# Kernel optimization log

Measured on AMD Instinct MI355X. Metric: run time of the kernel, lower is better.

## Reference

```python
import jax, jax.numpy as jnp
import numpy as np


def setup_inputs() -> dict:
    key = jax.random.key(0)
    k0, k1, k2, k3, k4 = jax.random.split(key, 5)
    T, B, I, H = 1024, 128, 256, 256
    x = jax.random.normal(k0, (T, B, I), dtype=jnp.float32)
    h0 = jax.random.normal(k1, (1, B, H), dtype=jnp.float32)
    # prepacked transposed weights, gate order [r|z|n] along the 3H axis
    wihT = jax.random.normal(k2, (I, 3 * H), dtype=jnp.float32) * 0.05
    whhT = jax.random.normal(k3, (H, 3 * H), dtype=jnp.float32) * 0.05
    b = jax.random.normal(k4, (3 * H,), dtype=jnp.float32) * 0.05  # fused b_ih + b_hh
    return {"x": x, "h0": h0, "wihT": wihT, "whhT": whhT, "b": b}


def reference(x, h0, wihT, whhT, b):
    # Single-layer GRU recurrence, matching the fused CUDA kernel math:
    #   r = sigmoid(x Wir + h Whr + b_r)
    #   z = sigmoid(x Wiz + h Whz + b_z)
    #   h' = (1 - z) * n + z * h
    H = h0.shape[-1]
    br, bz, bn = b[:H], b[H:2 * H], b[2 * H:]

    def step(h, xt):
        gi = xt @ wihT   # (B, 3H)
        gh = h @ whhT    # (B, 3H)
        r = jax.nn.sigmoid(gi[:, :H] + gh[:, :H] + br)
        z = jax.nn.sigmoid(gi[:, H:2 * H] + gh[:, H:2 * H] + bz)
        n = jnp.tanh(gi[:, 2 * H:] + bn + r * gh[:, 2 * H:])
        h_new = (1.0 - z) * n + z * h
        return h_new, None

    h_final, _ = jax.lax.scan(step, h0[0], x)  # scan over T
    return h_final[None]  # (1, B, H)
```

## Files before the change

kernel.cpp:

```cpp
#include <hip/hip_runtime.h>
#include <hip/hip_fp16.h>

#define TT 1024
#define BB 128
#define II 256
#define HH 256
#define NG 768

__device__ __align__(16) unsigned short g_xbf[(size_t)TT * BB * II];
__device__ __align__(16) unsigned short g_wihB[NG * II];
__device__ __align__(16) _Float16       g_gi[(size_t)TT * BB * NG];

typedef __attribute__((ext_vector_type(8))) short    bfrag;
typedef __attribute__((ext_vector_type(8))) _Float16 hfrag;
typedef __attribute__((ext_vector_type(4))) float    f32x4;

__device__ __forceinline__ unsigned short f2bf(float f) {
    unsigned u = __float_as_uint(f);
    return (unsigned short)((u + 0x7fffu + ((u >> 16) & 1u)) >> 16);
}

__global__ void cvt_x_kernel(const float* __restrict__ x) {
    const int n4 = TT * BB * II / 4;
    for (int i = blockIdx.x * blockDim.x + threadIdx.x; i < n4;
         i += gridDim.x * blockDim.x) {
        float4 v = reinterpret_cast<const float4*>(x)[i];
        ushort4 o;
        o.x = f2bf(v.x); o.y = f2bf(v.y); o.z = f2bf(v.z); o.w = f2bf(v.w);
        reinterpret_cast<ushort4*>(g_xbf)[i] = o;
    }
}

__global__ void cvt_wih_kernel(const float* __restrict__ wihT) {
    const int n = blockIdx.x;
    const int k = threadIdx.x;
    g_wihB[n * II + k] = f2bf(wihT[k * NG + n]);
}

__global__ void __launch_bounds__(256) gi_gemm_kernel(const float* __restrict__ bias) {
    __shared__ unsigned short Ab[128 * 32];
    __shared__ unsigned short Bb[128 * 32];
    const int tid = threadIdx.x;
    const int mt = blockIdx.x / 6, nt = blockIdx.x % 6;
    const int m0 = mt * 128, n0 = nt * 128;
    const int l = tid & 63, w = tid >> 6;
    const int wr = w >> 1, wc = w & 1;
    const int srow = tid >> 2, scol = (tid & 3) * 8;

    f32x4 acc[4][4] = {};

    for (int ks = 0; ks < 8; ++ks) {
        const int k0 = ks * 32;
        __syncthreads();
        #pragma unroll
        for (int c = 0; c < 2; ++c) {
            const int row = c * 64 + srow;
            *reinterpret_cast<uint4*>(&Ab[row * 32 + scol]) =
                *reinterpret_cast<const uint4*>(&g_xbf[(size_t)(m0 + row) * II + k0 + scol]);
            *reinterpret_cast<uint4*>(&Bb[row * 32 + scol]) =
                *reinterpret_cast<const uint4*>(&g_wihB[(n0 + row) * II + k0 + scol]);
        }
        __syncthreads();
        bfrag af[4], bf[4];
        #pragma unroll
        for (int i = 0; i < 4; ++i) {
            af[i] = *reinterpret_cast<const bfrag*>(
                        &Ab[(wr * 64 + i * 16 + (l & 15)) * 32 + (l >> 4) * 8]);
            bf[i] = *reinterpret_cast<const bfrag*>(
                        &Bb[(wc * 64 + i * 16 + (l & 15)) * 32 + (l >> 4) * 8]);
        }
        #pragma unroll
        for (int mi = 0; mi < 4; ++mi)
            #pragma unroll
            for (int ni = 0; ni < 4; ++ni)
                acc[mi][ni] = __builtin_amdgcn_mfma_f32_16x16x32_bf16(
                                  af[mi], bf[ni], acc[mi][ni], 0, 0, 0);
    }
    #pragma unroll
    for (int mi = 0; mi < 4; ++mi) {
        const int grow = m0 + wr * 64 + mi * 16 + (l >> 4) * 4;
        #pragma unroll
        for (int ni = 0; ni < 4; ++ni) {
            const int gcol = n0 + wc * 64 + ni * 16 + (l & 15);
            const float bv = bias[gcol];
            #pragma unroll
            for (int q = 0; q < 4; ++q)
                g_gi[(size_t)(grow + q) * NG + gcol] = (_Float16)(acc[mi][ni][q] + bv);
        }
    }
}

#define MF(A, B, C) __builtin_amdgcn_mfma_f32_16x16x32_f16((A), (B), (C), 0, 0, 0)

#define LDB1(NAME, CB, KT)                                                  \
    hfrag NAME;                                                             \
    _Pragma("unroll")                                                       \
    for (int e = 0; e < 8; ++e)                                             \
        NAME[e] = (_Float16)whhT[(size_t)((KT) * 32 + g8 + e) * NG + (CB) + c]; \
    asm("" : "+a"(NAME));

#define DECL8(P, CB)                                                        \
    LDB1(P##_0, CB, 0) LDB1(P##_1, CB, 1) LDB1(P##_2, CB, 2)                \
    LDB1(P##_3, CB, 3) LDB1(P##_4, CB, 4) LDB1(P##_5, CB, 5)                \
    LDB1(P##_6, CB, 6) LDB1(P##_7, CB, 7)

#define KST(KT)                                                             \
    {                                                                       \
        const hfrag A = *reinterpret_cast<const hfrag*>(hl + (KT) * 32 + g8); \
        aR0 = MF(A, BR0_##KT, aR0); aR1 = MF(A, BR1_##KT, aR1);             \
        aZ0 = MF(A, BZ0_##KT, aZ0); aZ1 = MF(A, BZ1_##KT, aZ1);             \
        aN0 = MF(A, BN0_##KT, aN0); aN1 = MF(A, BN1_##KT, aN1);             \
    }

__global__ void __launch_bounds__(512, 1) gru_rec_kernel(
    const float* __restrict__ h0, const float* __restrict__ whhT,
    float* __restrict__ out)
{
    __shared__ __align__(16) _Float16 hbuf[2][HH];

    const int t   = threadIdx.x;
    const int b   = blockIdx.x;
    const int w   = t >> 6;
    const int l   = t & 63;
    const int c   = l & 15;
    const int sel = l >> 4;
    const int g8  = sel * 8;
    const int cw  = w * 16;
    const int j   = (sel & 1) * 128 + cw + c;

    DECL8(BR0, cw)        DECL8(BR1, 128 + cw)
    DECL8(BZ0, 256 + cw)  DECL8(BZ1, 384 + cw)
    DECL8(BN0, 512 + cw)  DECL8(BN1, 640 + cw)

    float hp = h0[b * HH + j];
    hbuf[0][j] = (_Float16)hp;
    __syncthreads();

    for (int ts = 0; ts < TT; ++ts) {
        const _Float16* hl  = hbuf[ts & 1];
        _Float16*       hn_ = hbuf[(ts & 1) ^ 1];

        const _Float16* gb = g_gi + ((size_t)ts * BB + b) * NG + j;
        const float gR = (float)gb[0];
        const float gZ = (float)gb[256];
        const float gN = (float)gb[512];

        f32x4 aR0 = {0.f,0.f,0.f,0.f}, aR1 = {0.f,0.f,0.f,0.f};
        f32x4 aZ0 = {0.f,0.f,0.f,0.f}, aZ1 = {0.f,0.f,0.f,0.f};
        f32x4 aN0 = {0.f,0.f,0.f,0.f}, aN1 = {0.f,0.f,0.f,0.f};
        KST(0) KST(1) KST(2) KST(3) KST(4) KST(5) KST(6) KST(7)

        const float sR = (sel & 1) ? aR1[0] : aR0[0];
        const float sZ = (sel & 1) ? aZ1[0] : aZ0[0];
        const float sN = (sel & 1) ? aN1[0] : aN0[0];

        const float r  = 1.f / (1.f + __expf(-(sR + gR)));
        const float z  = 1.f / (1.f + __expf(-(sZ + gZ)));
        const float e  = __expf(2.f * (gN + r * sN));
        const float n  = 1.f - 2.f / (e + 1.f);
        const float hv = (1.f - z) * n + z * hp;

        hp = hv;
        hn_[j] = (_Float16)hv;
        if (ts == TT - 1) out[b * HH + j] = hv;
        __syncthreads();
    }
}

extern "C" void kernel_launch(void* const* d_in, const int* in_sizes, int n_in,
                              void* d_out, int out_size, void* d_ws, size_t ws_size,
                              hipStream_t stream) {
    const float* x    = (const float*)d_in[0];
    const float* h0   = (const float*)d_in[1];
    const float* wihT = (const float*)d_in[2];
    const float* whhT = (const float*)d_in[3];
    const float* bias = (const float*)d_in[4];
    float*       out  = (float*)d_out;

    cvt_x_kernel<<<2048, 256, 0, stream>>>(x);
    cvt_wih_kernel<<<NG, 256, 0, stream>>>(wihT);
    gi_gemm_kernel<<<1024 * 6, 256, 0, stream>>>(bias);
    gru_rec_kernel<<<BB, 512, 0, stream>>>(h0, whhT, out);
}
```

Before: 1.345 ms.

## Split recurrent GEMV across 16 waves with 1024-thread blocks

The recurrence kernel now launches 1024 threads per batch row, so each of 16 waves owns a single 16-column slice per gate instead of two. Each wave keeps half as many weight fragments in AGPRs and issues 24 MFMAs per step instead of 48, shortening the serial per-timestep critical path. In exchange the per-step __syncthreads covers twice as many waves, and only sel==0 lanes write the new hidden state, leaving the other lanes' results redundant.

Measured after the change: 2.869 ms. +113.3%, slower.

```diff
diff --git a/kernel.cpp b/kernel.cpp
--- a/kernel.cpp
+++ b/kernel.cpp
@@ -107,12 +107,12 @@
 #define KST(KT)                                                             \
     {                                                                       \
         const hfrag A = *reinterpret_cast<const hfrag*>(hl + (KT) * 32 + g8); \
-        aR0 = MF(A, BR0_##KT, aR0); aR1 = MF(A, BR1_##KT, aR1);             \
-        aZ0 = MF(A, BZ0_##KT, aZ0); aZ1 = MF(A, BZ1_##KT, aZ1);             \
-        aN0 = MF(A, BN0_##KT, aN0); aN1 = MF(A, BN1_##KT, aN1);             \
+        aR = MF(A, BR_##KT, aR);                                            \
+        aZ = MF(A, BZ_##KT, aZ);                                            \
+        aN = MF(A, BN_##KT, aN);                                            \
     }
 
-__global__ void __launch_bounds__(512, 1) gru_rec_kernel(
+__global__ void __launch_bounds__(1024, 1) gru_rec_kernel(
     const float* __restrict__ h0, const float* __restrict__ whhT,
     float* __restrict__ out)
 {
@@ -126,14 +126,14 @@
     const int sel = l >> 4;
     const int g8  = sel * 8;
     const int cw  = w * 16;
-    const int j   = (sel & 1) * 128 + cw + c;
+    const int j   = cw + c;
 
-    DECL8(BR0, cw)        DECL8(BR1, 128 + cw)
-    DECL8(BZ0, 256 + cw)  DECL8(BZ1, 384 + cw)
-    DECL8(BN0, 512 + cw)  DECL8(BN1, 640 + cw)
+    DECL8(BR, cw)
+    DECL8(BZ, 256 + cw)
+    DECL8(BN, 512 + cw)
 
     float hp = h0[b * HH + j];
-    hbuf[0][j] = (_Float16)hp;
+    if (sel == 0) hbuf[0][j] = (_Float16)hp;
     __syncthreads();
 
     for (int ts = 0; ts < TT; ++ts) {
@@ -145,24 +145,22 @@
         const float gZ = (float)gb[256];
         const float gN = (float)gb[512];
 
-        f32x4 aR0 = {0.f,0.f,0.f,0.f}, aR1 = {0.f,0.f,0.f,0.f};
-        f32x4 aZ0 = {0.f,0.f,0.f,0.f}, aZ1 = {0.f,0.f,0.f,0.f};
-        f32x4 aN0 = {0.f,0.f,0.f,0.f}, aN1 = {0.f,0.f,0.f,0.f};
+        f32x4 aR = {0.f,0.f,0.f,0.f};
+        f32x4 aZ = {0.f,0.f,0.f,0.f};
+        f32x4 aN = {0.f,0.f,0.f,0.f};
         KST(0) KST(1) KST(2) KST(3) KST(4) KST(5) KST(6) KST(7)
 
-        const float sR = (sel & 1) ? aR1[0] : aR0[0];
-        const float sZ = (sel & 1) ? aZ1[0] : aZ0[0];
-        const float sN = (sel & 1) ? aN1[0] : aN0[0];
-
-        const float r  = 1.f / (1.f + __expf(-(sR + gR)));
-        const float z  = 1.f / (1.f + __expf(-(sZ + gZ)));
-        const float e  = __expf(2.f * (gN + r * sN));
+        const float r  = 1.f / (1.f + __expf(-(aR[0] + gR)));
+        const float z  = 1.f / (1.f + __expf(-(aZ[0] + gZ)));
+        const float e  = __expf(2.f * (gN + r * aN[0]));
         const float n  = 1.f - 2.f / (e + 1.f);
         const float hv = (1.f - z) * n + z * hp;
 
         hp = hv;
-        hn_[j] = (_Float16)hv;
-        if (ts == TT - 1) out[b * HH + j] = hv;
+        if (sel == 0) {
+            hn_[j] = (_Float16)hv;
+            if (ts == TT - 1) out[b * HH + j] = hv;
+        }
         __syncthreads();
     }
 }
@@ -180,5 +178,5 @@
     cvt_x_kernel<<<2048, 256, 0, stream>>>(x);
     cvt_wih_kernel<<<NG, 256, 0, stream>>>(wihT);
     gi_gemm_kernel<<<1024 * 6, 256, 0, stream>>>(bias);
-    gru_rec_kernel<<<BB, 512, 0, stream>>>(h0, whhT, out);
+    gru_rec_kernel<<<BB, 1024, 0, stream>>>(h0, whhT, out);
 }
```
